# Kernel optimization log

Measured on AMD Instinct MI355X. Metric: run time of the kernel, lower is better.

Reference implementation:

```python
import jax, jax.numpy as jnp
import numpy as np

T, B, D, H = 256, 128, 1024, 1024


def setup_inputs() -> dict:
    key = jax.random.key(0)
    ks = jax.random.split(key, 9)
    s = 1.0 / np.sqrt(D + H)  # nn.Linear default init scale
    inp = {"inputs": jax.random.normal(ks[0], (T, B, D), dtype=jnp.float32)}
    names = ["Wf", "bf", "Wi", "bi", "Wg", "bg", "Wo", "bo"]
    for j, name in enumerate(names):
        shape = (H, D + H) if name.startswith("W") else (H,)
        inp[name] = jax.random.uniform(ks[j + 1], shape, jnp.float32, -s, s)
    return inp


def reference(inputs, Wf, bf, Wi, bi, Wg, bg, Wo, bo):
    # inputs: [T, B, D]; gate weights: [H, D+H] (torch Linear layout)
    b = inputs.shape[1]
    h = Wf.shape[0]
    hx0 = jnp.zeros((b, h), inputs.dtype)
    cx0 = jnp.zeros((b, h), inputs.dtype)

    def step(carry, x):
        hx, cx = carry
        z = jnp.concatenate([x, hx], axis=1)  # [B, D+H]
        f = jax.nn.sigmoid(z @ Wf.T + bf)
        i = jax.nn.sigmoid(z @ Wi.T + bi)
        g = jnp.tanh(z @ Wg.T + bg)
        o = jax.nn.sigmoid(z @ Wo.T + bo)
        cx = f * cx + i * g
        hx = o * jnp.tanh(cx)
        return (hx, cx), hx

    (hx, cx), outputs = jax.lax.scan(step, (hx0, cx0), inputs)
    return outputs, hx, cx
```

## Files before the change

### kernel.cpp

```cpp
#include <hip/hip_runtime.h>

typedef _Float16 h8 __attribute__((ext_vector_type(8)));
typedef _Float16 h4 __attribute__((ext_vector_type(4)));
typedef float    f4 __attribute__((ext_vector_type(4)));
typedef unsigned long long u64;

#define NBLK 256

__device__ __forceinline__ float sigm(float x) {
    return 1.0f / (1.0f + __expf(-x));
}
__device__ __forceinline__ float tanh_fast(float x) {
    return 1.0f - 2.0f / (__expf(2.0f * x) + 1.0f);
}

__device__ __forceinline__ void bar_arrive(unsigned* slot, int bid, unsigned barno) {
    __syncthreads();
    if (threadIdx.x == 0)
        __hip_atomic_store(&slot[bid * 64], barno + 1u, __ATOMIC_RELAXED,
                           __HIP_MEMORY_SCOPE_AGENT);
}
__device__ __forceinline__ void bar_wait(unsigned* slot, int mg, unsigned barno) {
    if (threadIdx.x < 64) {
        const unsigned tgt = barno + 1u;
        unsigned* p0 = &slot[(mg * 128 + threadIdx.x) * 64];
        unsigned* p1 = p0 + 64 * 64;
        unsigned spins = 0;
        float keep = (float)barno;
        for (;;) {
            unsigned v0 = __hip_atomic_load(p0, __ATOMIC_RELAXED,
                                            __HIP_MEMORY_SCOPE_AGENT);
            unsigned v1 = __hip_atomic_load(p1, __ATOMIC_RELAXED,
                                            __HIP_MEMORY_SCOPE_AGENT);
            if (__all(v0 >= tgt && v1 >= tgt)) break;
#pragma unroll
            for (int i = 0; i < 32; ++i)
                keep = __builtin_fmaf(keep, 1.0000001f, 1.0f);
            if (++spins > (1u << 22)) break;
        }
        asm volatile("" :: "v"(keep));
    }
    __syncthreads();
}

__global__ void prep_kernel(const float* __restrict__ x, _Float16* __restrict__ xbuf,
                            unsigned* __restrict__ ctr, unsigned* __restrict__ hb0u) {
    const int gtid = blockIdx.x * blockDim.x + threadIdx.x;
    if (gtid < 16384) ctr[gtid] = 0u;
    if (gtid < 65536) hb0u[gtid] = 0u;
    const f4* src = (const f4*)x;
    h4* dst = (h4*)xbuf;
    const int stride = gridDim.x * blockDim.x;
    for (int i = gtid; i < 8388608; i += stride)
        dst[i] = __builtin_convertvector(src[i], h4);
}

#define XHALF                                                                  \
    _Pragma("unroll")                                                          \
    for (int kc = 0; kc < 32; kc += 2) {                                       \
        h8 av0 = *(const h8*)(xA + kc * 32);                                   \
        h8 av1 = *(const h8*)(xA + kc * 32 + 32);                              \
        h8 b00 = *(const h8*)&wsm[kc * 1024 + boff];                           \
        h8 b10 = *(const h8*)&wsm[kc * 1024 + boff + 512];                     \
        h8 b01 = *(const h8*)&wsm[(kc + 1) * 1024 + boff];                     \
        h8 b11 = *(const h8*)&wsm[(kc + 1) * 1024 + boff + 512];               \
        a00 = __builtin_amdgcn_mfma_f32_16x16x32_f16(av0, b00, a00, 0, 0, 0);  \
        a10 = __builtin_amdgcn_mfma_f32_16x16x32_f16(av0, b10, a10, 0, 0, 0);  \
        a01 = __builtin_amdgcn_mfma_f32_16x16x32_f16(av1, b01, a01, 0, 0, 0);  \
        a11 = __builtin_amdgcn_mfma_f32_16x16x32_f16(av1, b11, a11, 0, 0, 0);  \
    }

#define LDH8(dst, elemoff)                                                     \
    do {                                                                       \
        union { u64 q[2]; h8 v; } u_;                                          \
        u64* p_ = (u64*)(hA + (elemoff));                                      \
        u_.q[0] = __hip_atomic_load(p_,     __ATOMIC_RELAXED,                  \
                                    __HIP_MEMORY_SCOPE_AGENT);                 \
        u_.q[1] = __hip_atomic_load(p_ + 1, __ATOMIC_RELAXED,                  \
                                    __HIP_MEMORY_SCOPE_AGENT);                 \
        dst = u_.v;                                                            \
    } while (0)

template<bool ROT>
__global__ __launch_bounds__(256, 1)
void lstm_kernel(const _Float16* __restrict__ xbuf,
                 _Float16* __restrict__ hb0, _Float16* __restrict__ hb1,
                 const float* __restrict__ Wf, const float* __restrict__ bfp,
                 const float* __restrict__ Wi, const float* __restrict__ bip,
                 const float* __restrict__ Wg, const float* __restrict__ bgp,
                 const float* __restrict__ Wo, const float* __restrict__ bop,
                 float* __restrict__ out,
                 unsigned* __restrict__ slot) {
    __shared__ _Float16 wsm[64 * 1024];

    const int tid = threadIdx.x;
    const int bid = blockIdx.x;
    const int mg = bid >> 7;
    const int ug = bid & 127;
    const int u0 = ug << 3;

    const float* WSEL[4] = {Wf, Wi, Wg, Wo};

    {
        const int col = tid & 31;
        const int kseg = tid >> 5;
        const float* srcp = WSEL[col >> 3] + (size_t)(u0 + (col & 7)) * 2048
                          + kseg * 256;
        const int cbase = (col >> 4) * 512 + (col & 15) * 8;
#pragma unroll 8
        for (int k4 = 0; k4 < 256; k4 += 4) {
            const int k = kseg * 256 + k4;
            f4 v = *(const f4*)(srcp + k4);
            h4 hv = __builtin_convertvector(v, h4);
            *(h4*)&wsm[(k >> 5) * 1024 + cbase + ((k >> 3) & 3) * 128 + (k & 7)] = hv;
        }
    }

    const int lane  = tid & 63;
    const int wv    = tid >> 6;
    const int row16 = lane & 15;
    const int quad  = lane >> 4;
    const int uu    = lane & 7;

    __syncthreads();

    const float bias_f = bfp[u0 + uu];
    const float bias_i = bip[u0 + uu];
    const float bias_g = bgp[u0 + uu];
    const float bias_o = bop[u0 + uu];

    const int zrow = mg * 64 + wv * 16 + row16;
    const int boff = quad * 128 + row16 * 8;
    const int drow = mg * 64 + wv * 16 + quad * 4;
    const bool writer = (lane & 8) == 0;
    const bool pstore = writer && ((uu & 1) == 0);
    const bool himask = (lane & 8) != 0;

    const _Float16* hbv[2] = {hb0, hb1};
    const size_t aoff = (size_t)zrow * 1024 + quad * 8;
    const _Float16* xbase = xbuf + aoff;
    const size_t obase = (size_t)drow * 1024 + u0 + uu;

    float cc[4] = {0.f, 0.f, 0.f, 0.f};
    float hnv[4];

    f4 a00 = {0.f,0.f,0.f,0.f}, a01 = {0.f,0.f,0.f,0.f};
    f4 a10 = {0.f,0.f,0.f,0.f}, a11 = {0.f,0.f,0.f,0.f};
    {
        const _Float16* xA = xbase;
        XHALF
    }

    for (int t = 0; t < 256; ++t) {
        if (t) bar_wait(slot, mg, (unsigned)(t - 1));

        const _Float16* hA = (ROT ? hb0 + (size_t)t * 131072 : hbv[t & 1]) + aoff;
        unsigned* hwu = (unsigned*)(ROT ? hb0 + (size_t)(t + 1) * 131072
                                        : hbv[(t + 1) & 1]);

#pragma unroll
        for (int kc = 32; kc < 64; kc += 2) {
            h8 av0, av1;
            if constexpr (ROT) {
                av0 = *(const h8*)(hA + (kc - 32) * 32);
                av1 = *(const h8*)(hA + (kc - 32) * 32 + 32);
            } else {
                LDH8(av0, (kc - 32) * 32);
                LDH8(av1, (kc - 32) * 32 + 32);
            }
            h8 b00 = *(const h8*)&wsm[kc * 1024 + boff];
            h8 b10 = *(const h8*)&wsm[kc * 1024 + boff + 512];
            h8 b01 = *(const h8*)&wsm[(kc + 1) * 1024 + boff];
            h8 b11 = *(const h8*)&wsm[(kc + 1) * 1024 + boff + 512];
            a00 = __builtin_amdgcn_mfma_f32_16x16x32_f16(av0, b00, a00, 0, 0, 0);
            a10 = __builtin_amdgcn_mfma_f32_16x16x32_f16(av0, b10, a10, 0, 0, 0);
            a01 = __builtin_amdgcn_mfma_f32_16x16x32_f16(av1, b01, a01, 0, 0, 0);
            a11 = __builtin_amdgcn_mfma_f32_16x16x32_f16(av1, b11, a11, 0, 0, 0);
        }

        f4 s0 = a00 + a01;
        f4 s1 = a10 + a11;
        float q0[4], q1[4];
#pragma unroll
        for (int j = 0; j < 4; ++j) {
            q0[j] = __shfl_xor(s0[j], 8, 64);
            q1[j] = __shfl_xor(s1[j], 8, 64);
        }
#pragma unroll
        for (int j = 0; j < 4; ++j) {
            float pf = himask ? q0[j] : s0[j];
            float pi = himask ? s0[j] : q0[j];
            float pg = himask ? q1[j] : s1[j];
            float po = himask ? s1[j] : q1[j];
            float fg = sigm(pf + bias_f);
            float ig = sigm(pi + bias_i);
            float gg = tanh_fast(pg + bias_g);
            float og = sigm(po + bias_o);
            float cn = fg * cc[j] + ig * gg;
            cc[j] = cn;
            float hn = og * tanh_fast(cn);
            hnv[j] = hn;
            float hp = __shfl_xor(hn, 1, 64);
            if (pstore) {
                _Float16 alo = (_Float16)hn, ahi = (_Float16)hp;
                unsigned short blo, bhi;
                __builtin_memcpy(&blo, &alo, 2);
                __builtin_memcpy(&bhi, &ahi, 2);
                unsigned pk = (unsigned)blo | ((unsigned)bhi << 16);
                __hip_atomic_store(&hwu[(obase >> 1) + (size_t)j * 512], pk,
                                   __ATOMIC_RELAXED, __HIP_MEMORY_SCOPE_AGENT);
            }
        }

        if (t < 255) {
            bar_arrive(slot, bid, (unsigned)t);
            if (writer) {
                float* outb = out + (size_t)t * 131072;
#pragma unroll
                for (int j = 0; j < 4; ++j)
                    __builtin_nontemporal_store(hnv[j], &outb[obase + (size_t)j * 1024]);
            }
            a00 = (f4){0.f,0.f,0.f,0.f}; a01 = (f4){0.f,0.f,0.f,0.f};
            a10 = (f4){0.f,0.f,0.f,0.f}; a11 = (f4){0.f,0.f,0.f,0.f};
            const _Float16* xA = xbase + (size_t)(t + 1) * 131072;
            XHALF
        } else if (writer) {
            float* outb = out + (size_t)255 * 131072;
#pragma unroll
            for (int j = 0; j < 4; ++j) {
                __builtin_nontemporal_store(hnv[j], &outb[obase + (size_t)j * 1024]);
                __builtin_nontemporal_store(hnv[j], &out[33554432 + obase + (size_t)j * 1024]);
            }
        }
    }
    if (writer) {
#pragma unroll
        for (int j = 0; j < 4; ++j)
            __builtin_nontemporal_store(
                cc[j], &out[33554432 + 131072 + obase + (size_t)j * 1024]);
    }
}

extern "C" void kernel_launch(void* const* d_in, const int* in_sizes, int n_in,
                              void* d_out, int out_size, void* d_ws, size_t ws_size,
                              hipStream_t stream) {
    const float* x  = (const float*)d_in[0];
    const float* Wf = (const float*)d_in[1];
    const float* bf = (const float*)d_in[2];
    const float* Wi = (const float*)d_in[3];
    const float* bi = (const float*)d_in[4];
    const float* Wg = (const float*)d_in[5];
    const float* bg = (const float*)d_in[6];
    const float* Wo = (const float*)d_in[7];
    const float* bo = (const float*)d_in[8];
    float* out = (float*)d_out;

    unsigned char* ws = (unsigned char*)d_ws;
    unsigned* slot = (unsigned*)ws;
    _Float16* hbase = (_Float16*)(ws + 65536);

    const size_t HROT = 257ull * 262144ull;
    const size_t ROT_NEED = 65536ull + HROT + 67108864ull;
    const bool rot = (ws_size >= ROT_NEED);

    _Float16* hb1  = (_Float16*)(ws + 65536 + 262144);
    _Float16* xbuf = rot ? (_Float16*)(ws + 65536 + HROT)
                         : (_Float16*)(ws + 65536 + 524288);

    prep_kernel<<<2048, 256, 0, stream>>>(x, xbuf, slot, (unsigned*)hbase);
    if (rot)
        lstm_kernel<true><<<NBLK, 256, 0, stream>>>(xbuf, hbase, hb1,
                                                    Wf, bf, Wi, bi, Wg, bg, Wo, bo,
                                                    out, slot);
    else
        lstm_kernel<false><<<NBLK, 256, 0, stream>>>(xbuf, hbase, hb1,
                                                     Wf, bf, Wi, bi, Wg, bg, Wo, bo,
                                                     out, slot);
}
```

Before: 3.219 ms.

## Split block into recurrent and input-projection waves with shared-memory handoff

Doubles the block to 512 threads. Four waves handle the recurrent h·W half and the gate math, while four new waves compute the next step's x·W projection in parallel and pass partial sums through shared memory. This takes the input projection off the serial critical path between grid barriers. The spin-wait now uses s_sleep instead of dummy FMAs. Costs are an extra __syncthreads per step and higher register and LDS pressure.

Result: faster. 2.655 ms (-17.5%).

```diff
diff --git a/kernel.cpp b/kernel.cpp
--- a/kernel.cpp
+++ b/kernel.cpp
@@ -12,35 +12,6 @@
 }
 __device__ __forceinline__ float tanh_fast(float x) {
     return 1.0f - 2.0f / (__expf(2.0f * x) + 1.0f);
-}
-
-__device__ __forceinline__ void bar_arrive(unsigned* slot, int bid, unsigned barno) {
-    __syncthreads();
-    if (threadIdx.x == 0)
-        __hip_atomic_store(&slot[bid * 64], barno + 1u, __ATOMIC_RELAXED,
-                           __HIP_MEMORY_SCOPE_AGENT);
-}
-__device__ __forceinline__ void bar_wait(unsigned* slot, int mg, unsigned barno) {
-    if (threadIdx.x < 64) {
-        const unsigned tgt = barno + 1u;
-        unsigned* p0 = &slot[(mg * 128 + threadIdx.x) * 64];
-        unsigned* p1 = p0 + 64 * 64;
-        unsigned spins = 0;
-        float keep = (float)barno;
-        for (;;) {
-            unsigned v0 = __hip_atomic_load(p0, __ATOMIC_RELAXED,
-                                            __HIP_MEMORY_SCOPE_AGENT);
-            unsigned v1 = __hip_atomic_load(p1, __ATOMIC_RELAXED,
-                                            __HIP_MEMORY_SCOPE_AGENT);
-            if (__all(v0 >= tgt && v1 >= tgt)) break;
-#pragma unroll
-            for (int i = 0; i < 32; ++i)
-                keep = __builtin_fmaf(keep, 1.0000001f, 1.0f);
-            if (++spins > (1u << 22)) break;
-        }
-        asm volatile("" :: "v"(keep));
-    }
-    __syncthreads();
 }
 
 __global__ void prep_kernel(const float* __restrict__ x, _Float16* __restrict__ xbuf,
@@ -82,7 +53,7 @@
     } while (0)
 
 template<bool ROT>
-__global__ __launch_bounds__(256, 1)
+__global__ __launch_bounds__(512, 1)
 void lstm_kernel(const _Float16* __restrict__ xbuf,
                  _Float16* __restrict__ hb0, _Float16* __restrict__ hb1,
                  const float* __restrict__ Wf, const float* __restrict__ bfp,
@@ -92,12 +63,16 @@
                  float* __restrict__ out,
                  unsigned* __restrict__ slot) {
     __shared__ _Float16 wsm[64 * 1024];
+    __shared__ float xp[4 * 64 * 8];
 
     const int tid = threadIdx.x;
     const int bid = blockIdx.x;
     const int mg = bid >> 7;
     const int ug = bid & 127;
     const int u0 = ug << 3;
+    const int wv8 = tid >> 6;
+    const bool hwave = wv8 < 4;
+    const int strip = wv8 & 3;
 
     const float* WSEL[4] = {Wf, Wi, Wg, Wo};
 
@@ -105,11 +80,11 @@
         const int col = tid & 31;
         const int kseg = tid >> 5;
         const float* srcp = WSEL[col >> 3] + (size_t)(u0 + (col & 7)) * 2048
-                          + kseg * 256;
+                          + kseg * 128;
         const int cbase = (col >> 4) * 512 + (col & 15) * 8;
 #pragma unroll 8
-        for (int k4 = 0; k4 < 256; k4 += 4) {
-            const int k = kseg * 256 + k4;
+        for (int k4 = 0; k4 < 128; k4 += 4) {
+            const int k = kseg * 128 + k4;
             f4 v = *(const f4*)(srcp + k4);
             h4 hv = __builtin_convertvector(v, h4);
             *(h4*)&wsm[(k >> 5) * 1024 + cbase + ((k >> 3) & 3) * 128 + (k & 7)] = hv;
@@ -117,7 +92,6 @@
     }
 
     const int lane  = tid & 63;
-    const int wv    = tid >> 6;
     const int row16 = lane & 15;
     const int quad  = lane >> 4;
     const int uu    = lane & 7;
@@ -129,9 +103,9 @@
     const float bias_g = bgp[u0 + uu];
     const float bias_o = bop[u0 + uu];
 
-    const int zrow = mg * 64 + wv * 16 + row16;
+    const int zrow = mg * 64 + strip * 16 + row16;
     const int boff = quad * 128 + row16 * 8;
-    const int drow = mg * 64 + wv * 16 + quad * 4;
+    const int drow = mg * 64 + strip * 16 + quad * 4;
     const bool writer = (lane & 8) == 0;
     const bool pstore = writer && ((uu & 1) == 0);
     const bool himask = (lane & 8) != 0;
@@ -140,91 +114,122 @@
     const size_t aoff = (size_t)zrow * 1024 + quad * 8;
     const _Float16* xbase = xbuf + aoff;
     const size_t obase = (size_t)drow * 1024 + u0 + uu;
+    const int xpb = (strip * 64 + lane) * 8;
 
     float cc[4] = {0.f, 0.f, 0.f, 0.f};
     float hnv[4];
 
     f4 a00 = {0.f,0.f,0.f,0.f}, a01 = {0.f,0.f,0.f,0.f};
     f4 a10 = {0.f,0.f,0.f,0.f}, a11 = {0.f,0.f,0.f,0.f};
-    {
+
+    if (!hwave) {
         const _Float16* xA = xbase;
         XHALF
+        *(f4*)&xp[xpb]     = a00 + a01;
+        *(f4*)&xp[xpb + 4] = a10 + a11;
     }
 
     for (int t = 0; t < 256; ++t) {
-        if (t) bar_wait(slot, mg, (unsigned)(t - 1));
-
-        const _Float16* hA = (ROT ? hb0 + (size_t)t * 131072 : hbv[t & 1]) + aoff;
-        unsigned* hwu = (unsigned*)(ROT ? hb0 + (size_t)(t + 1) * 131072
-                                        : hbv[(t + 1) & 1]);
-
-#pragma unroll
-        for (int kc = 32; kc < 64; kc += 2) {
-            h8 av0, av1;
-            if constexpr (ROT) {
-                av0 = *(const h8*)(hA + (kc - 32) * 32);
-                av1 = *(const h8*)(hA + (kc - 32) * 32 + 32);
-            } else {
-                LDH8(av0, (kc - 32) * 32);
-                LDH8(av1, (kc - 32) * 32 + 32);
-            }
-            h8 b00 = *(const h8*)&wsm[kc * 1024 + boff];
-            h8 b10 = *(const h8*)&wsm[kc * 1024 + boff + 512];
-            h8 b01 = *(const h8*)&wsm[(kc + 1) * 1024 + boff];
-            h8 b11 = *(const h8*)&wsm[(kc + 1) * 1024 + boff + 512];
-            a00 = __builtin_amdgcn_mfma_f32_16x16x32_f16(av0, b00, a00, 0, 0, 0);
-            a10 = __builtin_amdgcn_mfma_f32_16x16x32_f16(av0, b10, a10, 0, 0, 0);
-            a01 = __builtin_amdgcn_mfma_f32_16x16x32_f16(av1, b01, a01, 0, 0, 0);
-            a11 = __builtin_amdgcn_mfma_f32_16x16x32_f16(av1, b11, a11, 0, 0, 0);
-        }
-
-        f4 s0 = a00 + a01;
-        f4 s1 = a10 + a11;
-        float q0[4], q1[4];
-#pragma unroll
-        for (int j = 0; j < 4; ++j) {
-            q0[j] = __shfl_xor(s0[j], 8, 64);
-            q1[j] = __shfl_xor(s1[j], 8, 64);
-        }
-#pragma unroll
-        for (int j = 0; j < 4; ++j) {
-            float pf = himask ? q0[j] : s0[j];
-            float pi = himask ? s0[j] : q0[j];
-            float pg = himask ? q1[j] : s1[j];
-            float po = himask ? s1[j] : q1[j];
-            float fg = sigm(pf + bias_f);
-            float ig = sigm(pi + bias_i);
-            float gg = tanh_fast(pg + bias_g);
-            float og = sigm(po + bias_o);
-            float cn = fg * cc[j] + ig * gg;
-            cc[j] = cn;
-            float hn = og * tanh_fast(cn);
-            hnv[j] = hn;
-            float hp = __shfl_xor(hn, 1, 64);
-            if (pstore) {
-                _Float16 alo = (_Float16)hn, ahi = (_Float16)hp;
-                unsigned short blo, bhi;
-                __builtin_memcpy(&blo, &alo, 2);
-                __builtin_memcpy(&bhi, &ahi, 2);
-                unsigned pk = (unsigned)blo | ((unsigned)bhi << 16);
-                __hip_atomic_store(&hwu[(obase >> 1) + (size_t)j * 512], pk,
-                                   __ATOMIC_RELAXED, __HIP_MEMORY_SCOPE_AGENT);
-            }
-        }
-
-        if (t < 255) {
-            bar_arrive(slot, bid, (unsigned)t);
-            if (writer) {
-                float* outb = out + (size_t)t * 131072;
-#pragma unroll
-                for (int j = 0; j < 4; ++j)
-                    __builtin_nontemporal_store(hnv[j], &outb[obase + (size_t)j * 1024]);
-            }
+        if (t && tid < 64) {
+            const unsigned tgt = (unsigned)t;
+            unsigned* p0 = &slot[(mg * 128 + lane) * 64];
+            unsigned* p1 = p0 + 64 * 64;
+            unsigned spins = 0;
+            for (;;) {
+                unsigned v0 = __hip_atomic_load(p0, __ATOMIC_RELAXED,
+                                                __HIP_MEMORY_SCOPE_AGENT);
+                unsigned v1 = __hip_atomic_load(p1, __ATOMIC_RELAXED,
+                                                __HIP_MEMORY_SCOPE_AGENT);
+                if (__all(v0 >= tgt && v1 >= tgt)) break;
+                __builtin_amdgcn_s_sleep(2);
+                if (++spins > (1u << 24)) break;
+            }
+        }
+        __syncthreads();
+
+        if (hwave) {
+            const _Float16* hA = (ROT ? hb0 + (size_t)t * 131072 : hbv[t & 1]) + aoff;
+            unsigned* hwu = (unsigned*)(ROT ? hb0 + (size_t)(t + 1) * 131072
+                                            : hbv[(t + 1) & 1]);
+            a00 = (f4){0.f,0.f,0.f,0.f}; a01 = (f4){0.f,0.f,0.f,0.f};
+            a10 = (f4){0.f,0.f,0.f,0.f}; a11 = (f4){0.f,0.f,0.f,0.f};
+#pragma unroll
+            for (int kc = 32; kc < 64; kc += 2) {
+                h8 av0, av1;
+                if constexpr (ROT) {
+                    av0 = *(const h8*)(hA + (kc - 32) * 32);
+                    av1 = *(const h8*)(hA + (kc - 32) * 32 + 32);
+                } else {
+                    LDH8(av0, (kc - 32) * 32);
+                    LDH8(av1, (kc - 32) * 32 + 32);
+                }
+                h8 b00 = *(const h8*)&wsm[kc * 1024 + boff];
+                h8 b10 = *(const h8*)&wsm[kc * 1024 + boff + 512];
+                h8 b01 = *(const h8*)&wsm[(kc + 1) * 1024 + boff];
+                h8 b11 = *(const h8*)&wsm[(kc + 1) * 1024 + boff + 512];
+                a00 = __builtin_amdgcn_mfma_f32_16x16x32_f16(av0, b00, a00, 0, 0, 0);
+                a10 = __builtin_amdgcn_mfma_f32_16x16x32_f16(av0, b10, a10, 0, 0, 0);
+                a01 = __builtin_amdgcn_mfma_f32_16x16x32_f16(av1, b01, a01, 0, 0, 0);
+                a11 = __builtin_amdgcn_mfma_f32_16x16x32_f16(av1, b11, a11, 0, 0, 0);
+            }
+
+            f4 s0 = a00 + a01 + *(const f4*)&xp[xpb];
+            f4 s1 = a10 + a11 + *(const f4*)&xp[xpb + 4];
+            float q0[4], q1[4];
+#pragma unroll
+            for (int j = 0; j < 4; ++j) {
+                q0[j] = __shfl_xor(s0[j], 8, 64);
+                q1[j] = __shfl_xor(s1[j], 8, 64);
+            }
+#pragma unroll
+            for (int j = 0; j < 4; ++j) {
+                float pf = himask ? q0[j] : s0[j];
+                float pi = himask ? s0[j] : q0[j];
+                float pg = himask ? q1[j] : s1[j];
+                float po = himask ? s1[j] : q1[j];
+                float fg = sigm(pf + bias_f);
+                float ig = sigm(pi + bias_i);
+                float gg = tanh_fast(pg + bias_g);
+                float og = sigm(po + bias_o);
+                float cn = fg * cc[j] + ig * gg;
+                cc[j] = cn;
+                float hn = og * tanh_fast(cn);
+                hnv[j] = hn;
+                float hp = __shfl_xor(hn, 1, 64);
+                if (pstore) {
+                    _Float16 alo = (_Float16)hn, ahi = (_Float16)hp;
+                    unsigned short blo, bhi;
+                    __builtin_memcpy(&blo, &alo, 2);
+                    __builtin_memcpy(&bhi, &ahi, 2);
+                    unsigned pk = (unsigned)blo | ((unsigned)bhi << 16);
+                    __hip_atomic_store(&hwu[(obase >> 1) + (size_t)j * 512], pk,
+                                       __ATOMIC_RELAXED, __HIP_MEMORY_SCOPE_AGENT);
+                }
+            }
+        } else if (t < 255) {
             a00 = (f4){0.f,0.f,0.f,0.f}; a01 = (f4){0.f,0.f,0.f,0.f};
             a10 = (f4){0.f,0.f,0.f,0.f}; a11 = (f4){0.f,0.f,0.f,0.f};
             const _Float16* xA = xbase + (size_t)(t + 1) * 131072;
             XHALF
-        } else if (writer) {
+        }
+
+        __syncthreads();
+
+        if (!hwave && t < 255) {
+            *(f4*)&xp[xpb]     = a00 + a01;
+            *(f4*)&xp[xpb + 4] = a10 + a11;
+        }
+        if (t < 255) {
+            if (tid == 0)
+                __hip_atomic_store(&slot[bid * 64], (unsigned)(t + 1),
+                                   __ATOMIC_RELAXED, __HIP_MEMORY_SCOPE_AGENT);
+            if (hwave && writer) {
+                float* outb = out + (size_t)t * 131072;
+#pragma unroll
+                for (int j = 0; j < 4; ++j)
+                    __builtin_nontemporal_store(hnv[j], &outb[obase + (size_t)j * 1024]);
+            }
+        } else if (hwave && writer) {
             float* outb = out + (size_t)255 * 131072;
 #pragma unroll
             for (int j = 0; j < 4; ++j) {
@@ -233,7 +238,7 @@
             }
         }
     }
-    if (writer) {
+    if (hwave && writer) {
 #pragma unroll
         for (int j = 0; j < 4; ++j)
             __builtin_nontemporal_store(
@@ -269,11 +274,11 @@
 
     prep_kernel<<<2048, 256, 0, stream>>>(x, xbuf, slot, (unsigned*)hbase);
     if (rot)
-        lstm_kernel<true><<<NBLK, 256, 0, stream>>>(xbuf, hbase, hb1,
+        lstm_kernel<true><<<NBLK, 512, 0, stream>>>(xbuf, hbase, hb1,
                                                     Wf, bf, Wi, bi, Wg, bg, Wo, bo,
                                                     out, slot);
     else
-        lstm_kernel<false><<<NBLK, 256, 0, stream>>>(xbuf, hbase, hb1,
+        lstm_kernel<false><<<NBLK, 512, 0, stream>>>(xbuf, hbase, hb1,
                                                      Wf, bf, Wi, bi, Wg, bg, Wo, bo,
                                                      out, slot);
 }
```
